# Kernel optimization log

Hardware: AMD Instinct MI355X
Metric: run time of the kernel (lower is better)

The kernel has to match this reference:

```python
import jax, jax.numpy as jnp
import numpy as np

H = 32   # num_heads
G = 8    # num_groups (KV heads)
GS = H // G  # group_size
D_MODEL = 2048
HEAD_DIM = D_MODEL // H  # 64


def setup_inputs() -> dict:
    key = jax.random.key(0)
    ks = jax.random.split(key, 9)
    B, S = 2, 2048
    s_in = 1.0 / np.sqrt(D_MODEL)
    return {
        "x": jax.random.normal(ks[0], (B, S, D_MODEL), jnp.float32),
        "Wq": jax.random.normal(ks[1], (D_MODEL, H * HEAD_DIM), jnp.float32) * s_in,
        "bq": jnp.zeros((H * HEAD_DIM,), jnp.float32),
        "Wk": jax.random.normal(ks[2], (D_MODEL, G * HEAD_DIM), jnp.float32) * s_in,
        "bk": jnp.zeros((G * HEAD_DIM,), jnp.float32),
        "Wv": jax.random.normal(ks[3], (D_MODEL, G * HEAD_DIM), jnp.float32) * s_in,
        "bv": jnp.zeros((G * HEAD_DIM,), jnp.float32),
        "Wo": jax.random.normal(ks[4], (H * HEAD_DIM, D_MODEL), jnp.float32) * s_in,
        "bo": jnp.zeros((D_MODEL,), jnp.float32),
    }


def reference(x, Wq, bq, Wk, bk, Wv, bv, Wo, bo):
    B, S, _ = x.shape
    scale = 1.0 / np.sqrt(HEAD_DIM)
    # Projections
    q = (x @ Wq + bq).reshape(B, S, H, HEAD_DIM)          # [B,S,H,D]
    k = (x @ Wk + bk).reshape(B, S, G, HEAD_DIM)          # [B,S,G,D]
    v = (x @ Wv + bv).reshape(B, S, G, HEAD_DIM)
    # Group heads: head h belongs to group h // GS (matches repeat_interleave)
    q = q.reshape(B, S, G, GS, HEAD_DIM).transpose(0, 2, 3, 1, 4)  # [B,G,GS,S,D]
    k = k.transpose(0, 2, 1, 3)                                    # [B,G,S,D]
    v = v.transpose(0, 2, 1, 3)                                    # [B,G,S,D]
    # scores[b,g,m,s,t] = q[b,g,m,s,:] . k[b,g,t,:]
    scores = jnp.einsum('bgmsd,bgtd->bgmst', q, k) * scale
    attn = jax.nn.softmax(scores, axis=-1)
    ctx = jnp.einsum('bgmst,bgtd->bgmsd', attn, v)                 # [B,G,GS,S,D]
    ctx = ctx.transpose(0, 3, 1, 2, 4).reshape(B, S, H * HEAD_DIM)  # [B,S,d_model]
    return ctx @ Wo + bo
```

## Files before the change

kernel.cpp:

```cpp
#include <hip/hip_runtime.h>
#include <stdint.h>

#define DEVINL __device__ __forceinline__

typedef unsigned short u16;
typedef unsigned int   u32;
typedef __attribute__((ext_vector_type(8)))  __bf16 bf16x8;
typedef __attribute__((ext_vector_type(4)))  float  f32x4;
typedef __attribute__((ext_vector_type(16))) float  f32x16;
typedef __attribute__((ext_vector_type(4)))  u32    u32x4;

static constexpr int SEQ    = 2048;
static constexpr int DMODEL = 2048;
static constexpr int NHEAD  = 32;
static constexpr int NGRP   = 8;
static constexpr int DHEAD  = 64;
static constexpr int MTOK   = 2 * SEQ;
static constexpr int NQKV   = NHEAD*DHEAD + 2*NGRP*DHEAD;

DEVINL u16 f2bf(float f) {
  unsigned u = __builtin_bit_cast(unsigned, f);
  u += 0x7fffu + ((u >> 16) & 1u);
  return (u16)(u >> 16);
}

DEVINL void gld16(const void* g, void* l) {
  typedef __attribute__((address_space(1))) const void* gp_t;
  typedef __attribute__((address_space(3))) void* lp_t;
  __builtin_amdgcn_global_load_lds((gp_t)g, (lp_t)l, 16, 0, 0);
}

DEVINL f32x4 mfma16(bf16x8 a, bf16x8 b, f32x4 c) {
  return __builtin_amdgcn_mfma_f32_16x16x32_bf16(a, b, c, 0, 0, 0);
}
DEVINL f32x16 mfma32(bf16x8 a, bf16x8 b, f32x16 c) {
  return __builtin_amdgcn_mfma_f32_32x32x16_bf16(a, b, c, 0, 0, 0);
}
DEVINL u32 cvtpk(float lo, float hi_) {
  u32 r;
  asm("v_cvt_pk_bf16_f32 %0, %1, %2" : "=v"(r) : "v"(lo), "v"(hi_));
  return r;
}

__global__ void k_cvt(const float* __restrict__ s, u16* __restrict__ d) {
  int i = (blockIdx.x * 256 + threadIdx.x) * 4;
  float4 v = *reinterpret_cast<const float4*>(s + i);
  ushort4 o;
  o.x = f2bf(v.x); o.y = f2bf(v.y); o.z = f2bf(v.z); o.w = f2bf(v.w);
  *reinterpret_cast<ushort4*>(d + i) = o;
}

__global__ void k_tconv(const float* __restrict__ src, u16* __restrict__ dst, int N) {
  __shared__ float t[32][33];
  int n0 = blockIdx.x * 32, k0 = blockIdx.y * 32;
  int tx = threadIdx.x, ty = threadIdx.y;
  #pragma unroll
  for (int r = 0; r < 32; r += 8)
    t[r + ty][tx] = src[(size_t)(k0 + r + ty) * N + n0 + tx];
  __syncthreads();
  #pragma unroll
  for (int r = 0; r < 32; r += 8)
    dst[(size_t)(n0 + r + ty) * DMODEL + k0 + tx] = f2bf(t[tx][r + ty]);
}

__global__ void k_packbias(const float* __restrict__ bq, const float* __restrict__ bk,
                           const float* __restrict__ bv, float* __restrict__ d) {
  int i = blockIdx.x * 256 + threadIdx.x;
  d[i] = i < 2048 ? bq[i] : (i < 2560 ? bk[i - 2048] : bv[i - 2560]);
}

template<int ISV>
__global__ void k_pack(const u16* __restrict__ qkv, u16* __restrict__ out) {
  __shared__ u16 t[64][72];
  const int blk = blockIdx.x;
  const int sblk = blk & 31, g = (blk >> 5) & 7, bb = blk >> 8;
  const int tid = threadIdx.x;
  const size_t srcbase = ((size_t)bb * SEQ + sblk * 64) * NQKV + (ISV ? 2560 : 2048) + g * 64;
  #pragma unroll
  for (int i = 0; i < 2; ++i) {
    int c = tid * 2 + i;
    int row = c >> 3, dc = (c & 7) * 8;
    *(bf16x8*)&t[row][dc] = *(const bf16x8*)(qkv + srcbase + (size_t)row * NQKV + dc);
  }
  __syncthreads();
  const int bg = bb * 8 + g;
  #pragma unroll
  for (int r = 0; r < 2; ++r) {
    int f = tid + 256 * r;
    int lane = f & 63, cj = (f >> 6) & 3, stl = f >> 8;
    int q = lane & 31, hi = lane >> 5;
    size_t o = ((((size_t)bg * 64 + sblk * 2 + stl) * 4 + cj) * 64 + lane) * 8;
    if (ISV) {
      int dcol = (cj & 1) * 32 + q;
      int s0 = stl * 32 + (cj >> 1) * 16 + hi * 8;
      u16 tmp[8];
      #pragma unroll
      for (int e = 0; e < 8; ++e) tmp[e] = t[s0 + e][dcol];
      *(ushort4*)(out + o)     = *(ushort4*)&tmp[0];
      *(ushort4*)(out + o + 4) = *(ushort4*)&tmp[4];
    } else {
      int srow = stl * 32 + q;
      int d0 = cj * 16 + hi * 8;
      *(bf16x8*)(out + o) = *(const bf16x8*)&t[srow][d0];
    }
  }
}

template<int F32OUT>
__global__ __launch_bounds__(256, 3)
void k_gemm(const u16* __restrict__ A, const u16* __restrict__ Bt,
            const float* __restrict__ bias, void* __restrict__ Cv,
            int K, int ldc)
{
  __shared__ __align__(16) u16 lA[128 * 32];
  __shared__ __align__(16) u16 lB[128 * 32];
  const int tid = threadIdx.x;
  const int lane = tid & 63, wid = tid >> 6;
  const int fr = lane & 15, fq = lane >> 4;
  const int n0 = blockIdx.x * 128, m0 = blockIdx.y * 128;
  const int wr = wid >> 1, wc = wid & 1;

  f32x4 acc[4][4];
  #pragma unroll
  for (int i = 0; i < 4; ++i)
    #pragma unroll
    for (int j = 0; j < 4; ++j) acc[i][j] = f32x4{0.f, 0.f, 0.f, 0.f};

  const int s0 = (wid * 2 + 0) * 64 + lane;
  const int s1 = (wid * 2 + 1) * 64 + lane;
  const int r0 = s0 >> 2, k0s = 8 * (s0 & 3);
  const int r1 = s1 >> 2, k1s = 8 * (s1 & 3);
  const u16* gA0 = A  + (size_t)(m0 + r0) * K + k0s;
  const u16* gA1 = A  + (size_t)(m0 + r1) * K + k1s;
  const u16* gB0 = Bt + (size_t)(n0 + r0) * K + k0s;
  const u16* gB1 = Bt + (size_t)(n0 + r1) * K + k1s;
  u16* lA0 = &lA[(wid * 2 + 0) * 512];
  u16* lA1 = &lA[(wid * 2 + 1) * 512];
  u16* lB0 = &lB[(wid * 2 + 0) * 512];
  u16* lB1 = &lB[(wid * 2 + 1) * 512];

  int aoff[4], boff[4];
  #pragma unroll
  for (int i = 0; i < 4; ++i) {
    aoff[i] = (wr * 64 + i * 16 + fr) * 64 + fq * 16;
    boff[i] = (wc * 64 + i * 16 + fr) * 64 + fq * 16;
  }
  const char* laB = (const char*)lA;
  const char* lbB = (const char*)lB;

  for (int kt = 0; kt < K; kt += 32) {
    gld16(gA0, lA0); gld16(gA1, lA1);
    gld16(gB0, lB0); gld16(gB1, lB1);
    gA0 += 32; gA1 += 32; gB0 += 32; gB1 += 32;
    __syncthreads();
    bf16x8 a[4], b[4];
    #pragma unroll
    for (int i = 0; i < 4; ++i) a[i] = *(const bf16x8*)(laB + aoff[i]);
    #pragma unroll
    for (int j = 0; j < 4; ++j) b[j] = *(const bf16x8*)(lbB + boff[j]);
    #pragma unroll
    for (int i = 0; i < 4; ++i)
      #pragma unroll
      for (int j = 0; j < 4; ++j)
        acc[i][j] = mfma16(a[i], b[j], acc[i][j]);
    __syncthreads();
  }

  #pragma unroll
  for (int i = 0; i < 4; ++i) {
    const int row = m0 + wr * 64 + i * 16 + fq * 4;
    #pragma unroll
    for (int j = 0; j < 4; ++j) {
      const int col = n0 + wc * 64 + j * 16 + fr;
      const float bvl = bias[col];
      #pragma unroll
      for (int t = 0; t < 4; ++t) {
        const float val = acc[i][j][t] + bvl;
        if (F32OUT)
          ((float*)Cv)[(size_t)(row + t) * ldc + col] = val;
        else
          ((u16*)Cv)[(size_t)(row + t) * ldc + col] = f2bf(val);
      }
    }
  }
}

__global__ __launch_bounds__(256, 4)
void k_attn(const u16* __restrict__ qkv, const u16* __restrict__ kswz,
            const u16* __restrict__ vswz, u16* __restrict__ ctx)
{
  const int tid = threadIdx.x, lane = tid & 63, wid = tid >> 6;
  const int q = lane & 31, hi = lane >> 5;
  const int h = blockIdx.y, bb = blockIdx.z, g = h >> 2;
  const int qrow = blockIdx.x * 128 + wid * 32 + q;
  const size_t tokbase = (size_t)bb * SEQ;

  bf16x8 aq[4];
  {
    const u16* qp = qkv + (tokbase + qrow) * NQKV + h * 64 + hi * 8;
    #pragma unroll
    for (int c = 0; c < 4; ++c) aq[c] = *(const bf16x8*)(qp + 16 * c);
  }
  f32x16 o0, o1;
  #pragma unroll
  for (int r = 0; r < 16; ++r) { o0[r] = 0.f; o1[r] = 0.f; }
  float m = -3e38f, l = 0.f;

  const int bg = bb * 8 + g;
  const u16* kb = kswz + (size_t)bg * 131072 + lane * 8;
  const u16* vb = vswz + (size_t)bg * 131072 + lane * 8;

  const float cs  = 0.18033688011112042f;
  const float thr = 44.3614195558365f;

  bf16x8 kf[4];
  #pragma unroll
  for (int c = 0; c < 4; ++c) kf[c] = *(const bf16x8*)(kb + c * 512);

  for (int st = 0; st < SEQ / 32; ++st) {
    bf16x8 vf[4];
    #pragma unroll
    for (int j = 0; j < 4; ++j) vf[j] = *(const bf16x8*)(vb + (st * 4 + j) * 512);

    f32x16 s;
    #pragma unroll
    for (int r = 0; r < 16; ++r) s[r] = 0.f;
    __builtin_amdgcn_s_setprio(1);
    #pragma unroll
    for (int c = 0; c < 4; ++c) s = mfma32(kf[c], aq[c], s);
    __builtin_amdgcn_s_setprio(0);

    {
      const int sn = (st + 1 < SEQ / 32) ? st + 1 : 0;
      #pragma unroll
      for (int c = 0; c < 4; ++c) kf[c] = *(const bf16x8*)(kb + (sn * 4 + c) * 512);
    }

    float t8[8];
    #pragma unroll
    for (int r = 0; r < 8; ++r) t8[r] = fmaxf(s[r], s[r + 8]);
    float t4a = fmaxf(t8[0], t8[4]), t4b = fmaxf(t8[1], t8[5]);
    float t4c = fmaxf(t8[2], t8[6]), t4d = fmaxf(t8[3], t8[7]);
    float mx = fmaxf(fmaxf(t4a, t4b), fmaxf(t4c, t4d));
    mx = fmaxf(mx, __shfl_xor(mx, 32));

    if (!__all(mx - m <= thr)) {
      const float mn = fmaxf(m, mx);
      const float rs = exp2f((m - mn) * cs);
      m = mn; l *= rs;
      #pragma unroll
      for (int r = 0; r < 16; ++r) { o0[r] *= rs; o1[r] *= rs; }
    }

    const float mb = m * cs;
    float p[16];
    #pragma unroll
    for (int r = 0; r < 16; ++r) p[r] = exp2f(s[r] * cs - mb);
    float a8[8];
    #pragma unroll
    for (int r = 0; r < 8; ++r) a8[r] = p[r] + p[r + 8];
    float sum = ((a8[0] + a8[4]) + (a8[1] + a8[5])) + ((a8[2] + a8[6]) + (a8[3] + a8[7]));
    sum += __shfl_xor(sum, 32);
    l += sum;

    u32 w0 = cvtpk(p[0],  p[1]),  w1 = cvtpk(p[2],  p[3]);
    u32 w2 = cvtpk(p[4],  p[5]),  w3 = cvtpk(p[6],  p[7]);
    u32 w4 = cvtpk(p[8],  p[9]),  w5 = cvtpk(p[10], p[11]);
    u32 w6 = cvtpk(p[12], p[13]), w7 = cvtpk(p[14], p[15]);

    u32 cA = __shfl_xor(hi ? w0 : w2, 32);
    u32 cB = __shfl_xor(hi ? w1 : w3, 32);
    u32 cC = __shfl_xor(hi ? w4 : w6, 32);
    u32 cD = __shfl_xor(hi ? w5 : w7, 32);
    u32x4 t0, t1;
    t0.x = hi ? cA : w0;  t0.y = hi ? cB : w1;
    t0.z = hi ? w2 : cA;  t0.w = hi ? w3 : cB;
    t1.x = hi ? cC : w4;  t1.y = hi ? cD : w5;
    t1.z = hi ? w6 : cC;  t1.w = hi ? w7 : cD;
    bf16x8 pb0 = __builtin_bit_cast(bf16x8, t0);
    bf16x8 pb1 = __builtin_bit_cast(bf16x8, t1);

    __builtin_amdgcn_s_setprio(1);
    o0 = mfma32(vf[0], pb0, o0);
    o1 = mfma32(vf[1], pb0, o1);
    o0 = mfma32(vf[2], pb1, o0);
    o1 = mfma32(vf[3], pb1, o1);
    __builtin_amdgcn_s_setprio(0);
  }

  const float inv = 1.0f / l;
  u16* cp = ctx + (tokbase + qrow) * DMODEL + h * 64;
  #pragma unroll
  for (int t = 0; t < 4; ++t) {
    ushort4 oa, ob;
    oa.x = f2bf(o0[4*t+0] * inv); oa.y = f2bf(o0[4*t+1] * inv);
    oa.z = f2bf(o0[4*t+2] * inv); oa.w = f2bf(o0[4*t+3] * inv);
    *reinterpret_cast<ushort4*>(cp + 8*t + 4*hi) = oa;
    ob.x = f2bf(o1[4*t+0] * inv); ob.y = f2bf(o1[4*t+1] * inv);
    ob.z = f2bf(o1[4*t+2] * inv); ob.w = f2bf(o1[4*t+3] * inv);
    *reinterpret_cast<ushort4*>(cp + 32 + 8*t + 4*hi) = ob;
  }
}

extern "C" void kernel_launch(void* const* d_in, const int* in_sizes, int n_in,
                              void* d_out, int out_size, void* d_ws, size_t ws_size,
                              hipStream_t stream) {
  const float* x  = (const float*)d_in[0];
  const float* Wq = (const float*)d_in[1];
  const float* bq = (const float*)d_in[2];
  const float* Wk = (const float*)d_in[3];
  const float* bk = (const float*)d_in[4];
  const float* Wv = (const float*)d_in[5];
  const float* bv = (const float*)d_in[6];
  const float* Wo = (const float*)d_in[7];
  const float* bo = (const float*)d_in[8];

  char* ws = (char*)d_ws;
  size_t off = 0;
  auto take = [&](size_t bytes) { char* p = ws + off; off += (bytes + 255) & ~(size_t)255; return p; };
  u16*   xb    = (u16*)  take((size_t)MTOK * DMODEL * 2);
  u16*   wqkvT = (u16*)  take((size_t)NQKV * DMODEL * 2);
  u16*   woT   = (u16*)  take((size_t)DMODEL * DMODEL * 2);
  u16*   qkv   = (u16*)  take((size_t)MTOK * NQKV * 2);
  u16*   kswz  = (u16*)  take((size_t)16 * 131072 * 2);
  u16*   vswz  = (u16*)  take((size_t)16 * 131072 * 2);
  float* bqkv  = (float*)take((size_t)NQKV * 4);

  if (off > ws_size) {
    hipMemsetAsync(d_out, 0, (size_t)out_size * 4, stream);
    return;
  }

  dim3 tb(32, 8);
  k_cvt<<<(MTOK * DMODEL) / (4 * 256), 256, 0, stream>>>(x, xb);
  k_tconv<<<dim3(64, 64), tb, 0, stream>>>(Wq, wqkvT, 2048);
  k_tconv<<<dim3(16, 64), tb, 0, stream>>>(Wk, wqkvT + (size_t)2048 * DMODEL, 512);
  k_tconv<<<dim3(16, 64), tb, 0, stream>>>(Wv, wqkvT + (size_t)2560 * DMODEL, 512);
  k_tconv<<<dim3(64, 64), tb, 0, stream>>>(Wo, woT, 2048);
  k_packbias<<<NQKV / 256, 256, 0, stream>>>(bq, bk, bv, bqkv);

  k_gemm<0><<<dim3(NQKV / 128, MTOK / 128), 256, 0, stream>>>(
      xb, wqkvT, bqkv, qkv, DMODEL, NQKV);

  k_pack<0><<<512, 256, 0, stream>>>(qkv, kswz);
  k_pack<1><<<512, 256, 0, stream>>>(qkv, vswz);

  u16* ctxb = xb;
  k_attn<<<dim3(SEQ / 128, NHEAD, 2), 256, 0, stream>>>(qkv, kswz, vswz, ctxb);

  k_gemm<1><<<dim3(DMODEL / 128, MTOK / 128), 256, 0, stream>>>(
      ctxb, woT, bo, d_out, DMODEL, DMODEL);
}
```

Baseline: 262.5 us.

## Split KV sequence across wave pairs in attention and merge partials via LDS

Each attention block now handles 64 query rows, with pairs of waves splitting the KV sequence in half (split-K flash attention). The two partial softmax states are combined through shared memory at the end, which doubles the grid size and occupancy target. The cross-half P-fragment exchange now uses v_permlane32_swap instead of shuffles plus selects, and the row-max reduction is reordered. The cost is LDS traffic, a block barrier and a merge step, plus twice the Q loads per KV element.

```diff
diff --git a/kernel.cpp b/kernel.cpp
--- a/kernel.cpp
+++ b/kernel.cpp
@@ -40,6 +40,9 @@
   u32 r;
   asm("v_cvt_pk_bf16_f32 %0, %1, %2" : "=v"(r) : "v"(lo), "v"(hi_));
   return r;
+}
+DEVINL void plswap(u32& a, u32& b) {
+  asm("v_permlane32_swap_b32 %0, %1" : "+v"(a), "+v"(b));
 }
 
 __global__ void k_cvt(const float* __restrict__ s, u16* __restrict__ d) {
@@ -185,14 +188,17 @@
   }
 }
 
-__global__ __launch_bounds__(256, 4)
+__global__ __launch_bounds__(256, 6)
 void k_attn(const u16* __restrict__ qkv, const u16* __restrict__ kswz,
             const u16* __restrict__ vswz, u16* __restrict__ ctx)
 {
+  __shared__ float lm[2][64], ll[2][64];
+  __shared__ float lo[2][32][64];
   const int tid = threadIdx.x, lane = tid & 63, wid = tid >> 6;
   const int q = lane & 31, hi = lane >> 5;
+  const int qg = wid >> 1, kvh = wid & 1;
   const int h = blockIdx.y, bb = blockIdx.z, g = h >> 2;
-  const int qrow = blockIdx.x * 128 + wid * 32 + q;
+  const int qrow = blockIdx.x * 64 + qg * 32 + q;
   const size_t tokbase = (size_t)bb * SEQ;
 
   bf16x8 aq[4];
@@ -213,11 +219,13 @@
   const float cs  = 0.18033688011112042f;
   const float thr = 44.3614195558365f;
 
+  const int st0 = kvh * 32, st1 = st0 + 32;
+
   bf16x8 kf[4];
   #pragma unroll
-  for (int c = 0; c < 4; ++c) kf[c] = *(const bf16x8*)(kb + c * 512);
-
-  for (int st = 0; st < SEQ / 32; ++st) {
+  for (int c = 0; c < 4; ++c) kf[c] = *(const bf16x8*)(kb + (st0 * 4 + c) * 512);
+
+  for (int st = st0; st < st1; ++st) {
     bf16x8 vf[4];
     #pragma unroll
     for (int j = 0; j < 4; ++j) vf[j] = *(const bf16x8*)(vb + (st * 4 + j) * 512);
@@ -231,17 +239,17 @@
     __builtin_amdgcn_s_setprio(0);
 
     {
-      const int sn = (st + 1 < SEQ / 32) ? st + 1 : 0;
+      const int sn = (st + 1 < SEQ / 32) ? st + 1 : st;
       #pragma unroll
       for (int c = 0; c < 4; ++c) kf[c] = *(const bf16x8*)(kb + (sn * 4 + c) * 512);
     }
 
-    float t8[8];
-    #pragma unroll
-    for (int r = 0; r < 8; ++r) t8[r] = fmaxf(s[r], s[r + 8]);
-    float t4a = fmaxf(t8[0], t8[4]), t4b = fmaxf(t8[1], t8[5]);
-    float t4c = fmaxf(t8[2], t8[6]), t4d = fmaxf(t8[3], t8[7]);
-    float mx = fmaxf(fmaxf(t4a, t4b), fmaxf(t4c, t4d));
+    float m1 = fmaxf(fmaxf(s[0],  s[1]),  s[2]);
+    float m2 = fmaxf(fmaxf(s[3],  s[4]),  s[5]);
+    float m3 = fmaxf(fmaxf(s[6],  s[7]),  s[8]);
+    float m4 = fmaxf(fmaxf(s[9],  s[10]), s[11]);
+    float m5 = fmaxf(fmaxf(s[12], s[13]), s[14]);
+    float mx = fmaxf(fmaxf(fmaxf(fmaxf(m1, m2), m3), fmaxf(m4, m5)), s[15]);
     mx = fmaxf(mx, __shfl_xor(mx, 32));
 
     if (!__all(mx - m <= thr)) {
@@ -268,15 +276,11 @@
     u32 w4 = cvtpk(p[8],  p[9]),  w5 = cvtpk(p[10], p[11]);
     u32 w6 = cvtpk(p[12], p[13]), w7 = cvtpk(p[14], p[15]);
 
-    u32 cA = __shfl_xor(hi ? w0 : w2, 32);
-    u32 cB = __shfl_xor(hi ? w1 : w3, 32);
-    u32 cC = __shfl_xor(hi ? w4 : w6, 32);
-    u32 cD = __shfl_xor(hi ? w5 : w7, 32);
+    plswap(w0, w2);  plswap(w1, w3);
+    plswap(w4, w6);  plswap(w5, w7);
     u32x4 t0, t1;
-    t0.x = hi ? cA : w0;  t0.y = hi ? cB : w1;
-    t0.z = hi ? w2 : cA;  t0.w = hi ? w3 : cB;
-    t1.x = hi ? cC : w4;  t1.y = hi ? cD : w5;
-    t1.z = hi ? w6 : cC;  t1.w = hi ? w7 : cD;
+    t0.x = w0; t0.y = w1; t0.z = w2; t0.w = w3;
+    t1.x = w4; t1.y = w5; t1.z = w6; t1.w = w7;
     bf16x8 pb0 = __builtin_bit_cast(bf16x8, t0);
     bf16x8 pb1 = __builtin_bit_cast(bf16x8, t1);
 
@@ -288,17 +292,37 @@
     __builtin_amdgcn_s_setprio(0);
   }
 
-  const float inv = 1.0f / l;
-  u16* cp = ctx + (tokbase + qrow) * DMODEL + h * 64;
-  #pragma unroll
-  for (int t = 0; t < 4; ++t) {
-    ushort4 oa, ob;
-    oa.x = f2bf(o0[4*t+0] * inv); oa.y = f2bf(o0[4*t+1] * inv);
-    oa.z = f2bf(o0[4*t+2] * inv); oa.w = f2bf(o0[4*t+3] * inv);
-    *reinterpret_cast<ushort4*>(cp + 8*t + 4*hi) = oa;
-    ob.x = f2bf(o1[4*t+0] * inv); ob.y = f2bf(o1[4*t+1] * inv);
-    ob.z = f2bf(o1[4*t+2] * inv); ob.w = f2bf(o1[4*t+3] * inv);
-    *reinterpret_cast<ushort4*>(cp + 32 + 8*t + 4*hi) = ob;
+  if (kvh == 1) {
+    lm[qg][lane] = m;
+    ll[qg][lane] = l;
+    #pragma unroll
+    for (int r = 0; r < 16; ++r) {
+      lo[qg][r][lane]      = o0[r];
+      lo[qg][16 + r][lane] = o1[r];
+    }
+  }
+  __syncthreads();
+  if (kvh == 0) {
+    const float mp = lm[qg][lane], lp = ll[qg][lane];
+    const float mn = fmaxf(m, mp);
+    const float w1 = exp2f((m - mn) * cs);
+    const float w2 = exp2f((mp - mn) * cs);
+    const float inv = 1.0f / (l * w1 + lp * w2);
+    u16* cp = ctx + (tokbase + qrow) * DMODEL + h * 64;
+    #pragma unroll
+    for (int t = 0; t < 4; ++t) {
+      ushort4 oa, ob;
+      oa.x = f2bf((o0[4*t+0] * w1 + lo[qg][4*t+0][lane] * w2) * inv);
+      oa.y = f2bf((o0[4*t+1] * w1 + lo[qg][4*t+1][lane] * w2) * inv);
+      oa.z = f2bf((o0[4*t+2] * w1 + lo[qg][4*t+2][lane] * w2) * inv);
+      oa.w = f2bf((o0[4*t+3] * w1 + lo[qg][4*t+3][lane] * w2) * inv);
+      *reinterpret_cast<ushort4*>(cp + 8*t + 4*hi) = oa;
+      ob.x = f2bf((o1[4*t+0] * w1 + lo[qg][16+4*t+0][lane] * w2) * inv);
+      ob.y = f2bf((o1[4*t+1] * w1 + lo[qg][16+4*t+1][lane] * w2) * inv);
+      ob.z = f2bf((o1[4*t+2] * w1 + lo[qg][16+4*t+2][lane] * w2) * inv);
+      ob.w = f2bf((o1[4*t+3] * w1 + lo[qg][16+4*t+3][lane] * w2) * inv);
+      *reinterpret_cast<ushort4*>(cp + 32 + 8*t + 4*hi) = ob;
+    }
   }
 }
 
@@ -346,7 +370,7 @@
   k_pack<1><<<512, 256, 0, stream>>>(qkv, vswz);
 
   u16* ctxb = xb;
-  k_attn<<<dim3(SEQ / 128, NHEAD, 2), 256, 0, stream>>>(qkv, kswz, vswz, ctxb);
+  k_attn<<<dim3(SEQ / 64, NHEAD, 2), 256, 0, stream>>>(qkv, kswz, vswz, ctxb);
 
   k_gemm<1><<<dim3(DMODEL / 128, MTOK / 128), 256, 0, stream>>>(
       ctxb, woT, bo, d_out, DMODEL, DMODEL);
```

Result: slower. 735.9 us (+180.3%).
